# Kernel optimization log

Hardware: AMD Instinct MI355X
Metric: run time of the kernel (lower is better)

The kernel has to match this reference:

```python
import jax, jax.numpy as jnp
import numpy as np

N_NODES = 100000
N_EDGES = 1600000
NFEAT = 128
NHID = 128
NCLASS = 40
BN_EPS = 1e-5


def _glorot(key, shape):
    fan_in, fan_out = shape[1], shape[0]
    lim = (6.0 / (fan_in + fan_out)) ** 0.5
    return jax.random.uniform(key, shape, jnp.float32, -lim, lim)


def setup_inputs() -> dict:
    key = jax.random.key(0)
    ks = jax.random.split(key, 16)
    x = jax.random.normal(ks[0], (N_NODES, NFEAT), jnp.float32)
    src = jax.random.randint(ks[1], (N_EDGES,), 0, N_NODES, jnp.int64)
    dst = jax.random.randint(ks[2], (N_EDGES,), 0, N_NODES, jnp.int64)
    edge_index = jnp.stack([src, dst])  # [2, E]
    return {
        "x": x,
        "edge_index": edge_index,
        # conv1: nfeat -> nhid (lin_l with bias on aggregated msgs, lin_r no bias on root)
        "W1l": _glorot(ks[3], (NHID, NFEAT)), "b1": jnp.zeros((NHID,), jnp.float32),
        "W1r": _glorot(ks[4], (NHID, NFEAT)),
        # convx[0]: nhid -> nhid
        "Wxl": _glorot(ks[5], (NHID, NHID)), "bx": jnp.zeros((NHID,), jnp.float32),
        "Wxr": _glorot(ks[6], (NHID, NHID)),
        # conv2: nhid -> nclass
        "W2l": _glorot(ks[7], (NCLASS, NHID)), "b2": jnp.zeros((NCLASS,), jnp.float32),
        "W2r": _glorot(ks[8], (NCLASS, NHID)),
        # batch_norm3 (nhid) and batch_norm2 (nclass)
        "g3": jnp.ones((NHID,), jnp.float32), "be3": jnp.zeros((NHID,), jnp.float32),
        "g2": jnp.ones((NCLASS,), jnp.float32), "be2": jnp.zeros((NCLASS,), jnp.float32),
    }


def _sage_conv(x, src, dst, Wl, b, Wr):
    # mean aggregation of source features at destination nodes
    msg = x[src]                                                  # [E, F] gather
    agg = jax.ops.segment_sum(msg, dst, num_segments=N_NODES)    # [N, F] scatter-add
    cnt = jax.ops.segment_sum(jnp.ones((msg.shape[0],), x.dtype), dst, num_segments=N_NODES)
    mean = agg / jnp.maximum(cnt, 1.0)[:, None]                   # empty neighborhoods -> 0
    return mean @ Wl.T + b + x @ Wr.T


def _batch_norm(x, gamma, beta):
    mu = jnp.mean(x, axis=0)
    var = jnp.mean(jnp.square(x - mu), axis=0)  # biased var (training-mode BN)
    return (x - mu) * jax.lax.rsqrt(var + BN_EPS) * gamma + beta


def reference(x, edge_index, W1l, b1, W1r, Wxl, bx, Wxr, W2l, b2, W2r, g3, be3, g2, be2):
    src, dst = edge_index[0], edge_index[1]
    h = _sage_conv(x, src, dst, W1l, b1, W1r)      # conv1
    h = jax.nn.relu(h)
    # convx loop (nlayer - 2 == 1); dropout p=0 is identity
    h = _sage_conv(h, src, dst, Wxl, bx, Wxr)
    h = _batch_norm(h, g3, be3)                    # batch_norm3 (BN=True)
    h = jax.nn.relu(h)
    h = _sage_conv(h, src, dst, W2l, b2, W2r)      # conv2
    h = _batch_norm(h, g2, be2)                    # batch_norm2
    return h
```

## Files before the change

### kernel.cpp

```cpp
#include <hip/hip_runtime.h>
#include <hip/hip_bf16.h>

#define NN 100000
#define NE 1600000
#define NF 128
#define NC 40
#define BN_EPS 1e-5f

#define NB 256
#define NBU ((NN + 511) >> 9)
#define PT_TILE 4096
#define PT_GRID ((NE + PT_TILE - 1) / PT_TILE)
#define SBANK 32
#define NTILES (NN / 16)
#define LIN_GRID 1250
#define LIN80_GRID 512

typedef __attribute__((ext_vector_type(8))) short short8;
typedef __attribute__((ext_vector_type(4))) float float4v;
typedef __attribute__((ext_vector_type(4))) int int4v;

__device__ __forceinline__ unsigned short f2b(float f) {
    __hip_bfloat16 h = __float2bfloat16(f);
    return *reinterpret_cast<unsigned short*>(&h);
}
__device__ __forceinline__ float b2f_hi(unsigned u) { return __uint_as_float(u & 0xffff0000u); }
__device__ __forceinline__ float b2f_lo(unsigned u) { return __uint_as_float(u << 16); }


__global__ __launch_bounds__(256) void bhist_kernel(const int* __restrict__ dst,
                                                    int* __restrict__ bhist) {
    __shared__ int lh[NB];
    int tid = threadIdx.x;
    lh[tid] = 0;
    __syncthreads();
    int base = blockIdx.x * PT_TILE;
    int cnt = min(PT_TILE, NE - base);
    const int4v* d4 = (const int4v*)(dst + base);
    int cnt4 = cnt >> 2;
    for (int i = tid; i < cnt4; i += 256) {
        int4v d = __builtin_nontemporal_load(d4 + i);
        atomicAdd(&lh[d[0] >> 9], 1);
        atomicAdd(&lh[d[1] >> 9], 1);
        atomicAdd(&lh[d[2] >> 9], 1);
        atomicAdd(&lh[d[3] >> 9], 1);
    }
    __syncthreads();
    if (lh[tid]) atomicAdd(&bhist[tid], lh[tid]);
}

__global__ __launch_bounds__(256) void bscan_kernel(const int* __restrict__ bhist,
                                                    int* __restrict__ bbase,
                                                    int* __restrict__ bcur) {
    __shared__ int lds[NB];
    int t = threadIdx.x;
    int v = bhist[t];
    lds[t] = v;
    __syncthreads();
    for (int off = 1; off < NB; off <<= 1) {
        int u = (t >= off) ? lds[t - off] : 0;
        __syncthreads();
        lds[t] += u;
        __syncthreads();
    }
    int ex = lds[t] - v;
    bbase[t] = ex;
    bcur[t] = ex;
}

__global__ __launch_bounds__(256) void part_kernel(const int* __restrict__ src,
                                                   const int* __restrict__ dst,
                                                   int* __restrict__ bcur,
                                                   int2* __restrict__ stage) {
    __shared__ int2 pairs[PT_TILE];
    __shared__ int lhist[NB];
    __shared__ int gbase[NB];
    int tid = threadIdx.x;
    int base = blockIdx.x * PT_TILE;
    int cnt = min(PT_TILE, NE - base);
    int cnt4 = cnt >> 2;

    lhist[tid] = 0;
    __syncthreads();

    const int4v* d4 = (const int4v*)(dst + base);
    const int4v* s4 = (const int4v*)(src + base);
    for (int i = tid; i < cnt4; i += 256) {
        int4v d = __builtin_nontemporal_load(d4 + i);
        int4v s = __builtin_nontemporal_load(s4 + i);
#pragma unroll
        for (int j = 0; j < 4; ++j) {
            pairs[j * cnt4 + i] = make_int2(d[j], s[j]);
            atomicAdd(&lhist[d[j] >> 9], 1);
        }
    }
    __syncthreads();

    int c = lhist[tid];
    gbase[tid] = (c > 0) ? atomicAdd(&bcur[tid], c) : 0;
    lhist[tid] = 0;
    __syncthreads();

    for (int k = tid; k < cnt; k += 256) {
        int2 p = pairs[k];
        int b = p.x >> 9;
        int pos = atomicAdd(&lhist[b], 1);
        stage[gbase[b] + pos] = p;
    }
}

__global__ __launch_bounds__(256) void bucket_deg_kernel(const long long* __restrict__ stage,
                                                         const int* __restrict__ bbase,
                                                         const int* __restrict__ bcur,
                                                         int* __restrict__ deg) {
    int b = blockIdx.x;
    int s = bbase[b], e = bcur[b];
    for (int i = s + threadIdx.x; i < e; i += 256) {
        long long p = __builtin_nontemporal_load(stage + i);
        int d = (int)(p & 0xffffffffLL);
        atomicAdd(&deg[d], 1);
    }
}

__global__ __launch_bounds__(1024) void scan1_kernel(const int* __restrict__ deg,
                                                     int* __restrict__ row_loc,
                                                     int* __restrict__ blocksum) {
    __shared__ int lds[1024];
    int t = threadIdx.x;
    int i = blockIdx.x * 1024 + t;
    int v = (i < NN) ? deg[i] : 0;
    lds[t] = v;
    __syncthreads();
    for (int off = 1; off < 1024; off <<= 1) {
        int u = (t >= off) ? lds[t - off] : 0;
        __syncthreads();
        lds[t] += u;
        __syncthreads();
    }
    if (i < NN) row_loc[i] = lds[t] - v;
    if (t == 1023) blocksum[blockIdx.x] = lds[1023];
}

__global__ __launch_bounds__(128) void scan2_kernel(int* __restrict__ blocksum, int nb) {
    __shared__ int lds[128];
    int t = threadIdx.x;
    int v = (t < nb) ? blocksum[t] : 0;
    lds[t] = v;
    __syncthreads();
    for (int off = 1; off < 128; off <<= 1) {
        int u = (t >= off) ? lds[t - off] : 0;
        __syncthreads();
        lds[t] += u;
        __syncthreads();
    }
    if (t < nb) blocksum[t] = lds[t] - v;
}

__global__ __launch_bounds__(1024) void scan3_kernel(const int* __restrict__ deg,
                                                     const int* __restrict__ row_loc,
                                                     const int* __restrict__ blockoff,
                                                     int* __restrict__ row_ptr,
                                                     float* __restrict__ inv_cnt) {
    int i = blockIdx.x * 1024 + threadIdx.x;
    if (i < NN) {
        row_ptr[i] = blockoff[blockIdx.x] + row_loc[i];
        int d = deg[i];
        inv_cnt[i] = 1.0f / (float)(d > 0 ? d : 1);
    }
    if (i == 0) row_ptr[NN] = NE;
}

__global__ __launch_bounds__(256) void bucket_fill_kernel(const long long* __restrict__ stage,
                                                          const int* __restrict__ bbase,
                                                          const int* __restrict__ bcur,
                                                          const int* __restrict__ row_ptr,
                                                          int* __restrict__ cursor,
                                                          int* __restrict__ csr) {
    int b = blockIdx.x;
    int s = bbase[b], e = bcur[b];
    for (int i = s + threadIdx.x; i < e; i += 256) {
        long long p = __builtin_nontemporal_load(stage + i);
        int d = (int)(p & 0xffffffffLL);
        int sv = (int)(p >> 32);
        int pos = atomicAdd(&cursor[d], 1);
        csr[row_ptr[d] + pos] = sv;
    }
}


__global__ __launch_bounds__(256) void f2b4_kernel(const float* __restrict__ in,
                                                   unsigned short* __restrict__ out, int n4) {
    int i = blockIdx.x * 256 + threadIdx.x;
    if (i < n4) {
        float4 v = ((const float4*)in)[i];
        ushort4 o;
        o.x = f2b(v.x); o.y = f2b(v.y); o.z = f2b(v.z); o.w = f2b(v.w);
        ((ushort4*)out)[i] = o;
    }
}


__global__ __launch_bounds__(64) void pack_w_kernel(const float* __restrict__ Wl,
                                                    const float* __restrict__ Wr,
                                                    unsigned short* __restrict__ Bp) {
    int nt = blockIdx.x & 7;
    int kk = blockIdx.x >> 3;
    int lane = threadIdx.x;
    int n = nt * 16 + (lane & 15);
    int kb = kk * 32 + (lane >> 4) * 8;
    size_t base = ((size_t)(kk * 8 + nt) * 64 + lane) * 8;
#pragma unroll
    for (int j = 0; j < 8; ++j) {
        int k = kb + j;
        float v = (k < NF) ? Wl[(size_t)n * NF + k] : Wr[(size_t)n * NF + (k - NF)];
        Bp[base + j] = f2b(v);
    }
}

__global__ __launch_bounds__(64) void pack_w80_kernel(const float* __restrict__ Wl,
                                                      const float* __restrict__ Wr,
                                                      unsigned short* __restrict__ Bp) {
    int nt = blockIdx.x % 5;
    int kk = blockIdx.x / 5;
    int lane = threadIdx.x;
    int n = nt * 16 + (lane & 15);
    int kb = kk * 32 + (lane >> 4) * 8;
    size_t base = ((size_t)(kk * 5 + nt) * 64 + lane) * 8;
#pragma unroll
    for (int j = 0; j < 8; ++j) {
        int k = kb + j;
        float v = (n < NC) ? Wl[(size_t)n * NF + k] : Wr[(size_t)(n - NC) * NF + k];
        Bp[base + j] = f2b(v);
    }
}


__device__ __forceinline__ void acc8(float* a, uint4 u) {
    a[0] += b2f_lo(u.x); a[1] += b2f_hi(u.x);
    a[2] += b2f_lo(u.y); a[3] += b2f_hi(u.y);
    a[4] += b2f_lo(u.z); a[5] += b2f_hi(u.z);
    a[6] += b2f_lo(u.w); a[7] += b2f_hi(u.w);
}

__global__ __launch_bounds__(256) void agg_mean_bf16(const unsigned short* __restrict__ X,
                                                     const int* __restrict__ csr,
                                                     const int* __restrict__ row_ptr,
                                                     const float* __restrict__ inv_cnt,
                                                     unsigned short* __restrict__ out) {
    int tid = threadIdx.x;
    int lane = tid & 63;
    int wave = tid >> 6;
    int qw = lane >> 4;
    int sl = lane & 15;
    int n = blockIdx.x * 16 + wave * 4 + qw;
    if (n >= NN) return;
    int s = row_ptr[n], e = row_ptr[n + 1];
    int foff = sl * 8;

    float a[8];
#pragma unroll
    for (int j = 0; j < 8; ++j) a[j] = 0.f;

    int i = s;
    for (; i + 4 <= e; i += 4) {
        int s0 = csr[i], s1 = csr[i + 1], s2 = csr[i + 2], s3 = csr[i + 3];
        uint4 u0 = *(const uint4*)(X + (size_t)s0 * NF + foff);
        uint4 u1 = *(const uint4*)(X + (size_t)s1 * NF + foff);
        uint4 u2 = *(const uint4*)(X + (size_t)s2 * NF + foff);
        uint4 u3 = *(const uint4*)(X + (size_t)s3 * NF + foff);
        acc8(a, u0); acc8(a, u1); acc8(a, u2); acc8(a, u3);
    }
    for (; i < e; ++i) {
        uint4 u = *(const uint4*)(X + (size_t)csr[i] * NF + foff);
        acc8(a, u);
    }

    float ic = inv_cnt[n];
    uint4 o;
    o.x = (unsigned)f2b(a[0] * ic) | ((unsigned)f2b(a[1] * ic) << 16);
    o.y = (unsigned)f2b(a[2] * ic) | ((unsigned)f2b(a[3] * ic) << 16);
    o.z = (unsigned)f2b(a[4] * ic) | ((unsigned)f2b(a[5] * ic) << 16);
    o.w = (unsigned)f2b(a[6] * ic) | ((unsigned)f2b(a[7] * ic) << 16);
    *(uint4*)(out + (size_t)n * NF + foff) = o;
}


template <bool RELU, bool STATS>
__device__ __forceinline__ void lin_body(const unsigned short* __restrict__ Ab,
                                         const unsigned short* __restrict__ Xb,
                                         const unsigned short* __restrict__ Bp,
                                         const float* __restrict__ bias,
                                         unsigned short* __restrict__ outb,
                                         float* __restrict__ sums,
                                         float* ls) {
    int tid = threadIdx.x;
    int wave = tid >> 6;
    int lane = tid & 63;
    int quad = lane >> 4;
    int sl = lane & 15;
    const short8* Bv = (const short8*)Bp;

    if (STATS) {
        ls[tid] = 0.f;
        __syncthreads();
    }

    short8 bfr[8][2];
#pragma unroll
    for (int kk = 0; kk < 8; ++kk)
#pragma unroll
        for (int j = 0; j < 2; ++j)
            bfr[kk][j] = Bv[(kk * 8 + 2 * wave + j) * 64 + lane];

    float4 bias4[2];
#pragma unroll
    for (int j = 0; j < 2; ++j)
        bias4[j] = *(const float4*)(bias + (2 * wave + j) * 16 + quad * 4);

    float sts[2][4], stq[2][4];
    if (STATS) {
#pragma unroll
        for (int j = 0; j < 2; ++j)
#pragma unroll
            for (int r = 0; r < 4; ++r) { sts[j][r] = 0.f; stq[j][r] = 0.f; }
    }

    for (int t = blockIdx.x; t < NTILES; t += LIN_GRID) {
        int rr = t * 16 + sl;
        const unsigned short* arow = Ab + (size_t)rr * NF;
        const unsigned short* xrow = Xb + (size_t)rr * NF;

        short8 xf[8];
#pragma unroll
        for (int kk = 0; kk < 8; ++kk) {
            int kb = (kk & 3) * 32 + quad * 8;
            const unsigned short* asrc = (kk < 4) ? arow : xrow;
            xf[kk] = *(const short8*)(asrc + kb);
        }

        float4v acc[2];
#pragma unroll
        for (int j = 0; j < 2; ++j) acc[j] = (float4v){0.f, 0.f, 0.f, 0.f};

#pragma unroll
        for (int kk = 0; kk < 8; ++kk)
#pragma unroll
            for (int j = 0; j < 2; ++j)
                acc[j] = __builtin_amdgcn_mfma_f32_16x16x32_bf16(bfr[kk][j], xf[kk], acc[j], 0, 0, 0);

#pragma unroll
        for (int j = 0; j < 2; ++j) {
            int c0 = (2 * wave + j) * 16 + quad * 4;
            float v0 = acc[j][0] + bias4[j].x;
            float v1 = acc[j][1] + bias4[j].y;
            float v2 = acc[j][2] + bias4[j].z;
            float v3 = acc[j][3] + bias4[j].w;
            if (RELU) {
                v0 = fmaxf(v0, 0.f); v1 = fmaxf(v1, 0.f);
                v2 = fmaxf(v2, 0.f); v3 = fmaxf(v3, 0.f);
            }
            if (STATS) {
                sts[j][0] += v0; stq[j][0] += v0 * v0;
                sts[j][1] += v1; stq[j][1] += v1 * v1;
                sts[j][2] += v2; stq[j][2] += v2 * v2;
                sts[j][3] += v3; stq[j][3] += v3 * v3;
            }
            ushort4 o;
            o.x = f2b(v0); o.y = f2b(v1); o.z = f2b(v2); o.w = f2b(v3);
            *(ushort4*)(outb + (size_t)rr * NF + c0) = o;
        }
    }

    if (STATS) {
#pragma unroll
        for (int j = 0; j < 2; ++j) {
            int c0 = (2 * wave + j) * 16 + quad * 4;
#pragma unroll
            for (int r = 0; r < 4; ++r) {
                atomicAdd(&ls[c0 + r], sts[j][r]);
                atomicAdd(&ls[128 + c0 + r], stq[j][r]);
            }
        }
        __syncthreads();
        atomicAdd(&sums[(blockIdx.x & (SBANK - 1)) * 256 + tid], ls[tid]);
    }
}

__global__ __launch_bounds__(256, 3) void lin_conv1_kernel(const unsigned short* __restrict__ Ab,
                                                           const unsigned short* __restrict__ Xb,
                                                           const unsigned short* __restrict__ Bp,
                                                           const float* __restrict__ bias,
                                                           unsigned short* __restrict__ outb) {
    lin_body<true, false>(Ab, Xb, Bp, bias, outb, nullptr, nullptr);
}

__global__ __launch_bounds__(256, 3) void lin_convx_kernel(const unsigned short* __restrict__ Ab,
                                                           const unsigned short* __restrict__ Xb,
                                                           const unsigned short* __restrict__ Bp,
                                                           const float* __restrict__ bias,
                                                           unsigned short* __restrict__ outb,
                                                           float* __restrict__ sums) {
    __shared__ float ls[256];
    lin_body<false, true>(Ab, Xb, Bp, bias, outb, sums, ls);
}


__global__ __launch_bounds__(128) void bn3_coef_kernel(const float* __restrict__ sums,
                                                       const float* __restrict__ g,
                                                       const float* __restrict__ be,
                                                       float* __restrict__ sc,
                                                       float* __restrict__ sh) {
    int c = threadIdx.x;
    float sv = 0.f, qv = 0.f;
    for (int b = 0; b < SBANK; ++b) {
        sv += sums[b * 256 + c];
        qv += sums[b * 256 + 128 + c];
    }
    float invN = 1.0f / (float)NN;
    float mu = sv * invN;
    float var = qv * invN - mu * mu;
    float s = rsqrtf(var + BN_EPS) * g[c];
    sc[c] = s;
    sh[c] = be[c] - mu * s;
}


__global__ __launch_bounds__(256, 2) void lin80_mfma_kernel(const unsigned short* __restrict__ Xb,
                                                            const unsigned short* __restrict__ Bp,
                                                            const float* __restrict__ b2,
                                                            const float* __restrict__ bnsc,
                                                            const float* __restrict__ bnsh,
                                                            unsigned short* __restrict__ t40,
                                                            float* __restrict__ z40) {
    int tid = threadIdx.x;
    int wave = tid >> 6;
    int lane = tid & 63;
    int quad = lane >> 4;
    int sl = lane & 15;
    const short8* Bv = (const short8*)Bp;

    short8 bfr[4][5];
#pragma unroll
    for (int kk = 0; kk < 4; ++kk)
#pragma unroll
        for (int nt = 0; nt < 5; ++nt)
            bfr[kk][nt] = Bv[(kk * 5 + nt) * 64 + lane];

    float4 sc0[4], sc1[4], sh0[4], sh1[4];
#pragma unroll
    for (int kk = 0; kk < 4; ++kk) {
        int kb = kk * 32 + quad * 8;
        sc0[kk] = *(const float4*)(bnsc + kb);
        sc1[kk] = *(const float4*)(bnsc + kb + 4);
        sh0[kk] = *(const float4*)(bnsh + kb);
        sh1[kk] = *(const float4*)(bnsh + kb + 4);
    }

    int gw = blockIdx.x * 4 + wave;
    for (int t = gw; t < NTILES; t += LIN80_GRID * 4) {
        int rr = t * 16 + sl;
        const unsigned short* xrow = Xb + (size_t)rr * NF;

        float4v acc[5];
#pragma unroll
        for (int nt = 0; nt < 5; ++nt) acc[nt] = (float4v){0.f, 0.f, 0.f, 0.f};

#pragma unroll
        for (int kk = 0; kk < 4; ++kk) {
            uint4 u = *(const uint4*)(xrow + kk * 32 + quad * 8);
            short8 xf;
            xf[0] = (short)f2b(fmaxf(b2f_lo(u.x) * sc0[kk].x + sh0[kk].x, 0.f));
            xf[1] = (short)f2b(fmaxf(b2f_hi(u.x) * sc0[kk].y + sh0[kk].y, 0.f));
            xf[2] = (short)f2b(fmaxf(b2f_lo(u.y) * sc0[kk].z + sh0[kk].z, 0.f));
            xf[3] = (short)f2b(fmaxf(b2f_hi(u.y) * sc0[kk].w + sh0[kk].w, 0.f));
            xf[4] = (short)f2b(fmaxf(b2f_lo(u.z) * sc1[kk].x + sh1[kk].x, 0.f));
            xf[5] = (short)f2b(fmaxf(b2f_hi(u.z) * sc1[kk].y + sh1[kk].y, 0.f));
            xf[6] = (short)f2b(fmaxf(b2f_lo(u.w) * sc1[kk].z + sh1[kk].z, 0.f));
            xf[7] = (short)f2b(fmaxf(b2f_hi(u.w) * sc1[kk].w + sh1[kk].w, 0.f));
#pragma unroll
            for (int nt = 0; nt < 5; ++nt)
                acc[nt] = __builtin_amdgcn_mfma_f32_16x16x32_bf16(bfr[kk][nt], xf, acc[nt], 0, 0, 0);
        }

#pragma unroll
        for (int nt = 0; nt < 5; ++nt) {
            int c0 = nt * 16 + quad * 4;
            if (c0 < NC) {
                ushort4 o;
                o.x = f2b(acc[nt][0]); o.y = f2b(acc[nt][1]);
                o.z = f2b(acc[nt][2]); o.w = f2b(acc[nt][3]);
                *(ushort4*)(t40 + (size_t)rr * NC + c0) = o;
            } else {
                float4 bz = *(const float4*)(b2 + c0 - NC);
                float4 o;
                o.x = acc[nt][0] + bz.x; o.y = acc[nt][1] + bz.y;
                o.z = acc[nt][2] + bz.z; o.w = acc[nt][3] + bz.w;
                *(float4*)(z40 + (size_t)rr * NC + (c0 - NC)) = o;
            }
        }
    }
}


__global__ __launch_bounds__(256) void agg40_add_bf16(const unsigned short* __restrict__ T,
                                                      const float* __restrict__ Z,
                                                      const int* __restrict__ csr,
                                                      const int* __restrict__ row_ptr,
                                                      const float* __restrict__ inv_cnt,
                                                      float* __restrict__ out) {
    int tid = threadIdx.x;
    int lane = tid & 63;
    int wave = tid >> 6;
    if (lane >= 60) return;
    int sub = lane / 20;
    int sl = lane % 20;
    int n = blockIdx.x * 12 + wave * 3 + sub;
    if (n >= NN) return;
    int s = row_ptr[n], e = row_ptr[n + 1];
    const unsigned short* Tf = T + sl * 2;
    float a0 = 0.f, a1 = 0.f;
    int i = s;
    for (; i + 4 <= e; i += 4) {
        int s0 = csr[i], s1 = csr[i + 1], s2 = csr[i + 2], s3 = csr[i + 3];
        unsigned u0 = *(const unsigned*)(Tf + (size_t)s0 * NC);
        unsigned u1 = *(const unsigned*)(Tf + (size_t)s1 * NC);
        unsigned u2 = *(const unsigned*)(Tf + (size_t)s2 * NC);
        unsigned u3 = *(const unsigned*)(Tf + (size_t)s3 * NC);
        a0 += b2f_lo(u0) + b2f_lo(u1) + b2f_lo(u2) + b2f_lo(u3);
        a1 += b2f_hi(u0) + b2f_hi(u1) + b2f_hi(u2) + b2f_hi(u3);
    }
    for (; i < e; ++i) {
        unsigned u = *(const unsigned*)(Tf + (size_t)csr[i] * NC);
        a0 += b2f_lo(u);
        a1 += b2f_hi(u);
    }
    float ic = inv_cnt[n];
    const float2 zv = *(const float2*)(Z + (size_t)n * NC + sl * 2);
    float2 o;
    o.x = a0 * ic + zv.x;
    o.y = a1 * ic + zv.y;
    *(float2*)(out + (size_t)n * NC + sl * 2) = o;
}

#define BN_GRID 640

template <int F>
__global__ __launch_bounds__(256) void bn_stats2_kernel(const float* __restrict__ X,
                                                        float* __restrict__ sums) {
    __shared__ float ls[2 * F];
    int tid = threadIdx.x;
    for (int i = tid; i < 2 * F; i += 256) ls[i] = 0.f;
    __syncthreads();

    const int total4 = NN * F / 4;
    const int stride = BN_GRID * 256;
    int i0 = blockIdx.x * 256 + tid;
    int c0 = (i0 * 4) % F;
    float s0 = 0.f, s1 = 0.f, s2 = 0.f, s3 = 0.f;
    float q0 = 0.f, q1 = 0.f, q2 = 0.f, q3 = 0.f;
    for (int i = i0; i < total4; i += stride) {
        float4 v = ((const float4*)X)[i];
        s0 += v.x; q0 += v.x * v.x;
        s1 += v.y; q1 += v.y * v.y;
        s2 += v.z; q2 += v.z * v.z;
        s3 += v.w; q3 += v.w * v.w;
    }
    atomicAdd(&ls[c0 + 0], s0); atomicAdd(&ls[F + c0 + 0], q0);
    atomicAdd(&ls[c0 + 1], s1); atomicAdd(&ls[F + c0 + 1], q1);
    atomicAdd(&ls[c0 + 2], s2); atomicAdd(&ls[F + c0 + 2], q2);
    atomicAdd(&ls[c0 + 3], s3); atomicAdd(&ls[F + c0 + 3], q3);
    __syncthreads();
    for (int i = tid; i < 2 * F; i += 256) atomicAdd(&sums[i], ls[i]);
}

template <bool RELU>
__global__ __launch_bounds__(256) void bn_apply_kernel(float* __restrict__ X,
                                                       const float* __restrict__ sums,
                                                       const float* __restrict__ g,
                                                       const float* __restrict__ be,
                                                       int F, float invN) {
    size_t idx = (size_t)blockIdx.x * blockDim.x + threadIdx.x;
    size_t total = (size_t)NN * F;
    if (idx >= total) return;
    int t = (int)(idx % F);
    float mu = sums[t] * invN;
    float var = sums[F + t] * invN - mu * mu;
    float scale = rsqrtf(var + BN_EPS) * g[t];
    float v = (X[idx] - mu) * scale + be[t];
    if (RELU) v = fmaxf(v, 0.f);
    X[idx] = v;
}


extern "C" void kernel_launch(void* const* d_in, const int* in_sizes, int n_in,
                              void* d_out, int out_size, void* d_ws, size_t ws_size,
                              hipStream_t stream) {
    const float* x   = (const float*)d_in[0];
    const int*   ei  = (const int*)d_in[1];
    const int*   srcv = ei;
    const int*   dstv = ei + NE;
    const float* W1l = (const float*)d_in[2];
    const float* b1  = (const float*)d_in[3];
    const float* W1r = (const float*)d_in[4];
    const float* Wxl = (const float*)d_in[5];
    const float* bx  = (const float*)d_in[6];
    const float* Wxr = (const float*)d_in[7];
    const float* W2l = (const float*)d_in[8];
    const float* b2  = (const float*)d_in[9];
    const float* W2r = (const float*)d_in[10];
    const float* g3  = (const float*)d_in[11];
    const float* be3 = (const float*)d_in[12];
    const float* g2  = (const float*)d_in[13];
    const float* be2 = (const float*)d_in[14];
    float* out = (float*)d_out;

    char* w = (char*)d_ws;
    unsigned short* xb   = (unsigned short*)w; w += (size_t)NN * NF * 2;
    unsigned short* h1b  = (unsigned short*)w; w += (size_t)NN * NF * 2;
    unsigned short* aggb = (unsigned short*)w; w += (size_t)NN * NF * 2;
    unsigned short* h2b  = (unsigned short*)w; w += (size_t)NN * NF * 2;
    int* csr     = (int*)w; w += (size_t)NE * 4;
    int* row_ptr = (int*)w; w += (size_t)(NN + 4) * 4;
    int* deg     = (int*)w; w += (size_t)NN * 4;
    int* cursor  = (int*)w; w += (size_t)NN * 4;
    int* row_loc = (int*)w; w += (size_t)NN * 4;
    int* blocksum = (int*)w; w += 128 * 4;
    float* inv_cnt = (float*)w; w += (size_t)NN * 4;
    float* bnbuf3  = (float*)w; w += (size_t)SBANK * 256 * 4;
    float* bnbuf2  = (float*)w; w += 2 * NC * 4;
    float* bnsc    = (float*)w; w += NF * 4;
    float* bnsh    = (float*)w; w += NF * 4;
    unsigned short* Bp1 = (unsigned short*)w; w += (size_t)256 * NF * 2;
    unsigned short* Bpx = (unsigned short*)w; w += (size_t)256 * NF * 2;
    unsigned short* Bp2 = (unsigned short*)w; w += (size_t)128 * 80 * 2;
    int* bhist = (int*)w; w += NB * 4;
    int* bbase = (int*)w; w += NB * 4;
    int* bcurA = (int*)w; w += NB * 4;
    int2* stage = (int2*)h2b;
    unsigned short* t40 = xb;
    float* z40 = (float*)h1b;

    const int nscan = (NN + 1023) / 1024;

    hipMemsetAsync(deg, 0, (size_t)NN * 4, stream);
    hipMemsetAsync(cursor, 0, (size_t)NN * 4, stream);
    hipMemsetAsync(bhist, 0, NB * 4, stream);
    hipMemsetAsync(bnbuf3, 0, (size_t)SBANK * 256 * 4, stream);
    hipMemsetAsync(bnbuf2, 0, 2 * NC * 4, stream);

    bhist_kernel<<<PT_GRID, 256, 0, stream>>>(dstv, bhist);
    bscan_kernel<<<1, 256, 0, stream>>>(bhist, bbase, bcurA);
    part_kernel<<<PT_GRID, 256, 0, stream>>>(srcv, dstv, bcurA, stage);
    bucket_deg_kernel<<<NBU, 256, 0, stream>>>((const long long*)stage, bbase, bcurA, deg);
    scan1_kernel<<<nscan, 1024, 0, stream>>>(deg, row_loc, blocksum);
    scan2_kernel<<<1, 128, 0, stream>>>(blocksum, nscan);
    scan3_kernel<<<nscan, 1024, 0, stream>>>(deg, row_loc, blocksum, row_ptr, inv_cnt);
    bucket_fill_kernel<<<NBU, 256, 0, stream>>>((const long long*)stage, bbase, bcurA,
                                                row_ptr, cursor, csr);

    f2b4_kernel<<<(NN * NF / 4 + 255) / 256, 256, 0, stream>>>(x, xb, NN * NF / 4);
    pack_w_kernel<<<64, 64, 0, stream>>>(W1l, W1r, Bp1);
    pack_w_kernel<<<64, 64, 0, stream>>>(Wxl, Wxr, Bpx);
    pack_w80_kernel<<<20, 64, 0, stream>>>(W2l, W2r, Bp2);

    const int nblk_agg = (NN + 15) / 16;

    agg_mean_bf16<<<nblk_agg, 256, 0, stream>>>(xb, csr, row_ptr, inv_cnt, aggb);
    lin_conv1_kernel<<<LIN_GRID, 256, 0, stream>>>(aggb, xb, Bp1, b1, h1b);

    agg_mean_bf16<<<nblk_agg, 256, 0, stream>>>(h1b, csr, row_ptr, inv_cnt, aggb);
    lin_convx_kernel<<<LIN_GRID, 256, 0, stream>>>(aggb, h1b, Bpx, bx, h2b, bnbuf3);

    bn3_coef_kernel<<<1, 128, 0, stream>>>(bnbuf3, g3, be3, bnsc, bnsh);

    lin80_mfma_kernel<<<LIN80_GRID, 256, 0, stream>>>(h2b, Bp2, b2, bnsc, bnsh, t40, z40);
    agg40_add_bf16<<<(NN + 11) / 12, 256, 0, stream>>>(t40, z40, csr, row_ptr, inv_cnt, out);

    bn_stats2_kernel<NC><<<BN_GRID, 256, 0, stream>>>(out, bnbuf2);
    bn_apply_kernel<false><<<(NN * NC + 255) / 256, 256, 0, stream>>>(out, bnbuf2, g2, be2, NC, 1.0f / NN);
}
```

Measured before the change: 557.9 us.

## Fuse CSR degree, scan and fill into one per-bucket LDS kernel

Replaces the global-atomic degree count, three-kernel prefix scan and global-cursor fill with a single kernel per 512-node bucket. The kernel builds the local histogram, exclusive scan and insertion cursors in shared memory. This removes two memsets, four launches and global atomics on deg and cursor arrays. The aggregation inner loop is also rewritten to sum four neighbours before adding to the accumulator, which reorders the float additions.

```diff
diff --git a/kernel.cpp b/kernel.cpp
--- a/kernel.cpp
+++ b/kernel.cpp
@@ -109,81 +109,57 @@
     }
 }
 
-__global__ __launch_bounds__(256) void bucket_deg_kernel(const long long* __restrict__ stage,
-                                                         const int* __restrict__ bbase,
-                                                         const int* __restrict__ bcur,
-                                                         int* __restrict__ deg) {
+
+__global__ __launch_bounds__(512) void bucket_build_kernel(const long long* __restrict__ stage,
+                                                           const int* __restrict__ bbase,
+                                                           const int* __restrict__ bcur,
+                                                           int* __restrict__ row_ptr,
+                                                           float* __restrict__ inv_cnt,
+                                                           int* __restrict__ csr) {
+    __shared__ int hist[512];
+    __shared__ int sa[512], sb[512];
+    __shared__ int cur[512];
+    int tid = threadIdx.x;
     int b = blockIdx.x;
     int s = bbase[b], e = bcur[b];
-    for (int i = s + threadIdx.x; i < e; i += 256) {
+
+    hist[tid] = 0;
+    __syncthreads();
+
+    for (int i = s + tid; i < e; i += 512) {
         long long p = __builtin_nontemporal_load(stage + i);
-        int d = (int)(p & 0xffffffffLL);
-        atomicAdd(&deg[d], 1);
-    }
-}
-
-__global__ __launch_bounds__(1024) void scan1_kernel(const int* __restrict__ deg,
-                                                     int* __restrict__ row_loc,
-                                                     int* __restrict__ blocksum) {
-    __shared__ int lds[1024];
-    int t = threadIdx.x;
-    int i = blockIdx.x * 1024 + t;
-    int v = (i < NN) ? deg[i] : 0;
-    lds[t] = v;
-    __syncthreads();
-    for (int off = 1; off < 1024; off <<= 1) {
-        int u = (t >= off) ? lds[t - off] : 0;
+        int dl = ((int)(p & 0xffffffffLL)) & 511;
+        atomicAdd(&hist[dl], 1);
+    }
+    __syncthreads();
+
+    sa[tid] = hist[tid];
+    __syncthreads();
+    int* pin = sa;
+    int* pout = sb;
+    for (int off = 1; off < 512; off <<= 1) {
+        pout[tid] = pin[tid] + ((tid >= off) ? pin[tid - off] : 0);
         __syncthreads();
-        lds[t] += u;
-        __syncthreads();
-    }
-    if (i < NN) row_loc[i] = lds[t] - v;
-    if (t == 1023) blocksum[blockIdx.x] = lds[1023];
-}
-
-__global__ __launch_bounds__(128) void scan2_kernel(int* __restrict__ blocksum, int nb) {
-    __shared__ int lds[128];
-    int t = threadIdx.x;
-    int v = (t < nb) ? blocksum[t] : 0;
-    lds[t] = v;
-    __syncthreads();
-    for (int off = 1; off < 128; off <<= 1) {
-        int u = (t >= off) ? lds[t - off] : 0;
-        __syncthreads();
-        lds[t] += u;
-        __syncthreads();
-    }
-    if (t < nb) blocksum[t] = lds[t] - v;
-}
-
-__global__ __launch_bounds__(1024) void scan3_kernel(const int* __restrict__ deg,
-                                                     const int* __restrict__ row_loc,
-                                                     const int* __restrict__ blockoff,
-                                                     int* __restrict__ row_ptr,
-                                                     float* __restrict__ inv_cnt) {
-    int i = blockIdx.x * 1024 + threadIdx.x;
-    if (i < NN) {
-        row_ptr[i] = blockoff[blockIdx.x] + row_loc[i];
-        int d = deg[i];
-        inv_cnt[i] = 1.0f / (float)(d > 0 ? d : 1);
-    }
-    if (i == 0) row_ptr[NN] = NE;
-}
-
-__global__ __launch_bounds__(256) void bucket_fill_kernel(const long long* __restrict__ stage,
-                                                          const int* __restrict__ bbase,
-                                                          const int* __restrict__ bcur,
-                                                          const int* __restrict__ row_ptr,
-                                                          int* __restrict__ cursor,
-                                                          int* __restrict__ csr) {
-    int b = blockIdx.x;
-    int s = bbase[b], e = bcur[b];
-    for (int i = s + threadIdx.x; i < e; i += 256) {
+        int* t = pin; pin = pout; pout = t;
+    }
+
+    int d = hist[tid];
+    int ex = pin[tid] - d;
+    cur[tid] = ex;
+    int n = b * 512 + tid;
+    if (n < NN) {
+        row_ptr[n] = s + ex;
+        inv_cnt[n] = 1.0f / (float)(d > 0 ? d : 1);
+    }
+    if (b == 0 && tid == 0) row_ptr[NN] = NE;
+    __syncthreads();
+
+    for (int i = s + tid; i < e; i += 512) {
         long long p = __builtin_nontemporal_load(stage + i);
-        int d = (int)(p & 0xffffffffLL);
+        int dl = ((int)(p & 0xffffffffLL)) & 511;
         int sv = (int)(p >> 32);
-        int pos = atomicAdd(&cursor[d], 1);
-        csr[row_ptr[d] + pos] = sv;
+        int pos = atomicAdd(&cur[dl], 1);
+        csr[s + pos] = sv;
     }
 }
 
@@ -235,13 +211,6 @@
 }
 
 
-__device__ __forceinline__ void acc8(float* a, uint4 u) {
-    a[0] += b2f_lo(u.x); a[1] += b2f_hi(u.x);
-    a[2] += b2f_lo(u.y); a[3] += b2f_hi(u.y);
-    a[4] += b2f_lo(u.z); a[5] += b2f_hi(u.z);
-    a[6] += b2f_lo(u.w); a[7] += b2f_hi(u.w);
-}
-
 __global__ __launch_bounds__(256) void agg_mean_bf16(const unsigned short* __restrict__ X,
                                                      const int* __restrict__ csr,
                                                      const int* __restrict__ row_ptr,
@@ -268,11 +237,21 @@
         uint4 u1 = *(const uint4*)(X + (size_t)s1 * NF + foff);
         uint4 u2 = *(const uint4*)(X + (size_t)s2 * NF + foff);
         uint4 u3 = *(const uint4*)(X + (size_t)s3 * NF + foff);
-        acc8(a, u0); acc8(a, u1); acc8(a, u2); acc8(a, u3);
+        a[0] += b2f_lo(u0.x) + b2f_lo(u1.x) + b2f_lo(u2.x) + b2f_lo(u3.x);
+        a[1] += b2f_hi(u0.x) + b2f_hi(u1.x) + b2f_hi(u2.x) + b2f_hi(u3.x);
+        a[2] += b2f_lo(u0.y) + b2f_lo(u1.y) + b2f_lo(u2.y) + b2f_lo(u3.y);
+        a[3] += b2f_hi(u0.y) + b2f_hi(u1.y) + b2f_hi(u2.y) + b2f_hi(u3.y);
+        a[4] += b2f_lo(u0.z) + b2f_lo(u1.z) + b2f_lo(u2.z) + b2f_lo(u3.z);
+        a[5] += b2f_hi(u0.z) + b2f_hi(u1.z) + b2f_hi(u2.z) + b2f_hi(u3.z);
+        a[6] += b2f_lo(u0.w) + b2f_lo(u1.w) + b2f_lo(u2.w) + b2f_lo(u3.w);
+        a[7] += b2f_hi(u0.w) + b2f_hi(u1.w) + b2f_hi(u2.w) + b2f_hi(u3.w);
     }
     for (; i < e; ++i) {
         uint4 u = *(const uint4*)(X + (size_t)csr[i] * NF + foff);
-        acc8(a, u);
+        a[0] += b2f_lo(u.x); a[1] += b2f_hi(u.x);
+        a[2] += b2f_lo(u.y); a[3] += b2f_hi(u.y);
+        a[4] += b2f_lo(u.z); a[5] += b2f_hi(u.z);
+        a[6] += b2f_lo(u.w); a[7] += b2f_hi(u.w);
     }
 
     float ic = inv_cnt[n];
@@ -621,10 +600,6 @@
     unsigned short* h2b  = (unsigned short*)w; w += (size_t)NN * NF * 2;
     int* csr     = (int*)w; w += (size_t)NE * 4;
     int* row_ptr = (int*)w; w += (size_t)(NN + 4) * 4;
-    int* deg     = (int*)w; w += (size_t)NN * 4;
-    int* cursor  = (int*)w; w += (size_t)NN * 4;
-    int* row_loc = (int*)w; w += (size_t)NN * 4;
-    int* blocksum = (int*)w; w += 128 * 4;
     float* inv_cnt = (float*)w; w += (size_t)NN * 4;
     float* bnbuf3  = (float*)w; w += (size_t)SBANK * 256 * 4;
     float* bnbuf2  = (float*)w; w += 2 * NC * 4;
@@ -640,10 +615,6 @@
     unsigned short* t40 = xb;
     float* z40 = (float*)h1b;
 
-    const int nscan = (NN + 1023) / 1024;
-
-    hipMemsetAsync(deg, 0, (size_t)NN * 4, stream);
-    hipMemsetAsync(cursor, 0, (size_t)NN * 4, stream);
     hipMemsetAsync(bhist, 0, NB * 4, stream);
     hipMemsetAsync(bnbuf3, 0, (size_t)SBANK * 256 * 4, stream);
     hipMemsetAsync(bnbuf2, 0, 2 * NC * 4, stream);
@@ -651,12 +622,8 @@
     bhist_kernel<<<PT_GRID, 256, 0, stream>>>(dstv, bhist);
     bscan_kernel<<<1, 256, 0, stream>>>(bhist, bbase, bcurA);
     part_kernel<<<PT_GRID, 256, 0, stream>>>(srcv, dstv, bcurA, stage);
-    bucket_deg_kernel<<<NBU, 256, 0, stream>>>((const long long*)stage, bbase, bcurA, deg);
-    scan1_kernel<<<nscan, 1024, 0, stream>>>(deg, row_loc, blocksum);
-    scan2_kernel<<<1, 128, 0, stream>>>(blocksum, nscan);
-    scan3_kernel<<<nscan, 1024, 0, stream>>>(deg, row_loc, blocksum, row_ptr, inv_cnt);
-    bucket_fill_kernel<<<NBU, 256, 0, stream>>>((const long long*)stage, bbase, bcurA,
-                                                row_ptr, cursor, csr);
+    bucket_build_kernel<<<NBU, 512, 0, stream>>>((const long long*)stage, bbase, bcurA,
+                                                 row_ptr, inv_cnt, csr);
 
     f2b4_kernel<<<(NN * NF / 4 + 255) / 256, 256, 0, stream>>>(x, xb, NN * NF / 4);
     pack_w_kernel<<<64, 64, 0, stream>>>(W1l, W1r, Bp1);
```

Result: faster. 481.9 us (-13.6%).
